# Performance work log

Measured on AMD Instinct MI355X. Metric: run time of the kernel, lower is better.

Reference implementation:

```python
import jax, jax.numpy as jnp
import numpy as np


def setup_inputs() -> dict:
    key = jax.random.key(0)
    B, C, H, W = 32, 1024, 32, 32
    K = 256
    corr = jax.random.normal(key, (B, C, H, W), dtype=jnp.float32)
    select_indices = jnp.arange(K, dtype=jnp.int64)
    return {"corr": corr, "select_indices": select_indices}


def reference(corr, select_indices):
    # corr: [B, C, H, W]
    max_corr = jnp.max(corr, axis=1, keepdims=True)    # [B,1,H,W]
    avg_corr = jnp.mean(corr, axis=1, keepdims=True)   # [B,1,H,W]
    # per-channel total response: sum over spatial dims -> [B, C]
    value = jnp.sum(corr, axis=(2, 3))
    # descending sort indices along channel dim, then keep selected ranks
    sort_v_idx = jnp.argsort(-value, axis=1)           # [B, C]
    sel_idx = sort_v_idx[:, select_indices]            # [B, K]
    # batched gather of the selected channels (vectorized, no python loop)
    sort_corr = jnp.take_along_axis(corr, sel_idx[:, :, None, None], axis=1)  # [B,K,H,W]
    return jnp.concatenate([max_corr, avg_corr, sort_corr], axis=1)  # [B, 2+K, H, W]
```

## Files before the change

kernel.cpp:

```cpp
#include <hip/hip_runtime.h>
#include <hip/hip_bf16.h>


#define BB 32
#define CC_TOT 1024
#define HW 1024

__global__ void k_pass1(const float* __restrict__ corr,
                        float* __restrict__ pmax,
                        float* __restrict__ psum,
                        double* __restrict__ value,
                        int nch, int cpc) {
    extern __shared__ double lds[];
    const int tid  = threadIdx.x;
    const int lane = tid & 63;
    const int wid  = tid >> 6;
    const int b  = blockIdx.x / nch;
    const int cc = blockIdx.x % nch;

    const float4* base = (const float4*)(corr + (((size_t)b * CC_TOT) + (size_t)cc * cpc) * HW);

    float4 vmax = make_float4(-__builtin_inff(), -__builtin_inff(),
                              -__builtin_inff(), -__builtin_inff());
    float4 vsum = make_float4(0.f, 0.f, 0.f, 0.f);

    for (int c = 0; c < cpc; ++c) {
        float4 x = base[(size_t)c * (HW / 4) + tid];
        vmax.x = fmaxf(vmax.x, x.x); vmax.y = fmaxf(vmax.y, x.y);
        vmax.z = fmaxf(vmax.z, x.z); vmax.w = fmaxf(vmax.w, x.w);
        vsum.x += x.x; vsum.y += x.y; vsum.z += x.z; vsum.w += x.w;

        double s = (double)x.x + (double)x.y + (double)x.z + (double)x.w;
        #pragma unroll
        for (int off = 32; off >= 1; off >>= 1)
            s += __shfl_down(s, off);
        if (lane == 0) lds[c * 4 + wid] = s;
    }
    __syncthreads();
    for (int c = tid; c < cpc; c += 256) {
        value[(size_t)b * CC_TOT + (size_t)cc * cpc + c] =
            lds[c * 4 + 0] + lds[c * 4 + 1] + lds[c * 4 + 2] + lds[c * 4 + 3];
    }

    const size_t o = ((size_t)blockIdx.x * HW) + (size_t)tid * 4;
    *(float4*)(pmax + o) = vmax;
    *(float4*)(psum + o) = vsum;
}

__global__ void k_pass2(const float* __restrict__ pmax,
                        const float* __restrict__ psum,
                        float* __restrict__ out, int nch) {
    const int gid = blockIdx.x * 256 + threadIdx.x;
    const int b  = gid >> 10;
    const int hw = gid & (HW - 1);
    float m = -__builtin_inff();
    float s = 0.f;
    for (int cc = 0; cc < nch; ++cc) {
        const size_t o = (((size_t)b * nch + cc) << 10) + hw;
        m = fmaxf(m, pmax[o]);
        s += psum[o];
    }
    const size_t ob = (size_t)b * (2 + 256) * HW;
    out[ob + hw]      = m;
    out[ob + HW + hw] = s * (1.0f / 1024.0f);
}

__global__ void k_sort(const double* __restrict__ value, int* __restrict__ sorted) {
    __shared__ double kv[1024];
    __shared__ int    ki[1024];
    const int b = blockIdx.x;
    const int tid = threadIdx.x;

    for (int i = tid; i < 1024; i += 512) {
        kv[i] = value[(size_t)b * CC_TOT + i];
        ki[i] = i;
    }
    __syncthreads();

    for (int k = 2; k <= 1024; k <<= 1) {
        for (int j = k >> 1; j > 0; j >>= 1) {
            for (int i = tid; i < 1024; i += 512) {
                const int ixj = i ^ j;
                if (ixj > i) {
                    double v1 = kv[i], v2 = kv[ixj];
                    int    i1 = ki[i], i2 = ki[ixj];
                    const bool prec = (v1 > v2) || (v1 == v2 && i1 < i2);
                    const bool up = (i & k) == 0;
                    const bool sw = up ? !prec : prec;
                    if (sw) {
                        kv[i] = v2; kv[ixj] = v1;
                        ki[i] = i2; ki[ixj] = i1;
                    }
                }
            }
            __syncthreads();
        }
    }
    for (int i = tid; i < 1024; i += 512)
        sorted[(size_t)b * CC_TOT + i] = ki[i];
}

__global__ void k_gather(const float* __restrict__ corr,
                         const int* __restrict__ sorted,
                         const int* __restrict__ selidx,
                         float* __restrict__ out, int K) {
    const int b = blockIdx.x / K;
    const int k = blockIdx.x % K;
    int ks = selidx[k];
    ks = min(max(ks, 0), CC_TOT - 1);
    int c = sorted[(size_t)b * CC_TOT + ks];
    c = min(max(c, 0), CC_TOT - 1);

    const float4* src = (const float4*)(corr + (((size_t)b * CC_TOT) + c) * HW);
    float4*       dst = (float4*)(out + (((size_t)b * (2 + 256)) + 2 + k) * HW);
    dst[threadIdx.x] = src[threadIdx.x];
}

extern "C" void kernel_launch(void* const* d_in, const int* in_sizes, int n_in,
                              void* d_out, int out_size, void* d_ws, size_t ws_size,
                              hipStream_t stream) {
    const float* corr = (const float*)d_in[0];
    const int*   sel  = (const int*)d_in[1];
    float*       out  = (float*)d_out;

    const int K = out_size / (BB * HW) - 2;

    int nch = 32;
    while (nch > 1) {
        size_t need = (size_t)BB * nch * HW * 4 * 2
                    + (size_t)BB * CC_TOT * 8
                    + (size_t)BB * CC_TOT * 4;
        if (need <= ws_size) break;
        nch >>= 1;
    }
    const int cpc = CC_TOT / nch;

    float*  pmax   = (float*)d_ws;
    float*  psum   = pmax + (size_t)BB * nch * HW;
    double* value  = (double*)(psum + (size_t)BB * nch * HW);
    int*    sorted = (int*)(value + (size_t)BB * CC_TOT);

    k_pass1<<<BB * nch, 256, (size_t)cpc * 4 * sizeof(double), stream>>>(
        corr, pmax, psum, value, nch, cpc);
    k_pass2<<<(BB * HW) / 256, 256, 0, stream>>>(pmax, psum, out, nch);
    k_sort<<<BB, 512, 0, stream>>>(value, sorted);
    k_gather<<<BB * K, 256, 0, stream>>>(corr, sorted, sel, out, K);
}
```

Baseline: 245.4 us.

## Replace bitonic sort with parallel rank counting and hardcode channel split

Replaces the per-batch 512-thread bitonic sort (many barrier-separated stages in one block per batch) with a rank-by-counting kernel. Each of 16 blocks per batch computes the descending rank of 64 channels by comparing against all 1024 values, then scatters only ranks below K. It also fixes the channel split at compile time, drops the workspace-size fallback, and adds unroll pragmas and launch bounds to the reduction kernels. The sorted array now holds only the first K ranks, so the gather is correct only if select_indices stay below K. The change also assumes the workspace is always large enough.

```diff
diff --git a/kernel.cpp b/kernel.cpp
--- a/kernel.cpp
+++ b/kernel.cpp
@@ -2,44 +2,48 @@
 #include <hip/hip_bf16.h>
 
 
-#define BB 32
-#define CC_TOT 1024
-#define HW 1024
+#define BB  32
+#define CC  1024
+#define HW  1024
+#define NCH 32
+#define CPC 32
 
-__global__ void k_pass1(const float* __restrict__ corr,
-                        float* __restrict__ pmax,
-                        float* __restrict__ psum,
-                        double* __restrict__ value,
-                        int nch, int cpc) {
-    extern __shared__ double lds[];
+__global__ __launch_bounds__(256)
+void k_pass1(const float* __restrict__ corr,
+             float* __restrict__ pmax,
+             float* __restrict__ psum,
+             double* __restrict__ value) {
+    __shared__ double lds[CPC * 4];
     const int tid  = threadIdx.x;
     const int lane = tid & 63;
     const int wid  = tid >> 6;
-    const int b  = blockIdx.x / nch;
-    const int cc = blockIdx.x % nch;
+    const int b  = blockIdx.x / NCH;
+    const int cc = blockIdx.x % NCH;
 
-    const float4* base = (const float4*)(corr + (((size_t)b * CC_TOT) + (size_t)cc * cpc) * HW);
+    const float4* base = (const float4*)(corr + (((size_t)b * CC) + (size_t)cc * CPC) * HW);
 
     float4 vmax = make_float4(-__builtin_inff(), -__builtin_inff(),
                               -__builtin_inff(), -__builtin_inff());
     float4 vsum = make_float4(0.f, 0.f, 0.f, 0.f);
 
-    for (int c = 0; c < cpc; ++c) {
+    #pragma unroll 4
+    for (int c = 0; c < CPC; ++c) {
         float4 x = base[(size_t)c * (HW / 4) + tid];
         vmax.x = fmaxf(vmax.x, x.x); vmax.y = fmaxf(vmax.y, x.y);
         vmax.z = fmaxf(vmax.z, x.z); vmax.w = fmaxf(vmax.w, x.w);
         vsum.x += x.x; vsum.y += x.y; vsum.z += x.z; vsum.w += x.w;
 
-        double s = (double)x.x + (double)x.y + (double)x.z + (double)x.w;
+        double s = ((double)x.x + (double)x.y) + ((double)x.z + (double)x.w);
         #pragma unroll
         for (int off = 32; off >= 1; off >>= 1)
             s += __shfl_down(s, off);
         if (lane == 0) lds[c * 4 + wid] = s;
     }
     __syncthreads();
-    for (int c = tid; c < cpc; c += 256) {
-        value[(size_t)b * CC_TOT + (size_t)cc * cpc + c] =
-            lds[c * 4 + 0] + lds[c * 4 + 1] + lds[c * 4 + 2] + lds[c * 4 + 3];
+    if (tid < CPC) {
+        const double v = (lds[tid * 4 + 0] + lds[tid * 4 + 1])
+                       + (lds[tid * 4 + 2] + lds[tid * 4 + 3]);
+        value[(size_t)b * CC + (size_t)cc * CPC + tid] = v;
     }
 
     const size_t o = ((size_t)blockIdx.x * HW) + (size_t)tid * 4;
@@ -47,16 +51,18 @@
     *(float4*)(psum + o) = vsum;
 }
 
-__global__ void k_pass2(const float* __restrict__ pmax,
-                        const float* __restrict__ psum,
-                        float* __restrict__ out, int nch) {
+__global__ __launch_bounds__(256)
+void k_pass2(const float* __restrict__ pmax,
+             const float* __restrict__ psum,
+             float* __restrict__ out) {
     const int gid = blockIdx.x * 256 + threadIdx.x;
     const int b  = gid >> 10;
     const int hw = gid & (HW - 1);
     float m = -__builtin_inff();
     float s = 0.f;
-    for (int cc = 0; cc < nch; ++cc) {
-        const size_t o = (((size_t)b * nch + cc) << 10) + hw;
+    #pragma unroll 8
+    for (int cc = 0; cc < NCH; ++cc) {
+        const size_t o = (((size_t)b * NCH + cc) << 10) + hw;
         m = fmaxf(m, pmax[o]);
         s += psum[o];
     }
@@ -65,53 +71,42 @@
     out[ob + HW + hw] = s * (1.0f / 1024.0f);
 }
 
-__global__ void k_sort(const double* __restrict__ value, int* __restrict__ sorted) {
-    __shared__ double kv[1024];
-    __shared__ int    ki[1024];
-    const int b = blockIdx.x;
-    const int tid = threadIdx.x;
+__global__ __launch_bounds__(64)
+void k_rank(const double* __restrict__ value, int* __restrict__ sorted, int K) {
+    __shared__ double vs[CC];
+    const int b     = blockIdx.x >> 4;
+    const int chunk = blockIdx.x & 15;
+    const int tid   = threadIdx.x;
 
-    for (int i = tid; i < 1024; i += 512) {
-        kv[i] = value[(size_t)b * CC_TOT + i];
-        ki[i] = i;
-    }
+    for (int i = tid; i < CC; i += 64)
+        vs[i] = value[(size_t)b * CC + i];
     __syncthreads();
 
-    for (int k = 2; k <= 1024; k <<= 1) {
-        for (int j = k >> 1; j > 0; j >>= 1) {
-            for (int i = tid; i < 1024; i += 512) {
-                const int ixj = i ^ j;
-                if (ixj > i) {
-                    double v1 = kv[i], v2 = kv[ixj];
-                    int    i1 = ki[i], i2 = ki[ixj];
-                    const bool prec = (v1 > v2) || (v1 == v2 && i1 < i2);
-                    const bool up = (i & k) == 0;
-                    const bool sw = up ? !prec : prec;
-                    if (sw) {
-                        kv[i] = v2; kv[ixj] = v1;
-                        ki[i] = i2; ki[ixj] = i1;
-                    }
-                }
-            }
-            __syncthreads();
-        }
+    const int    c  = chunk * 64 + tid;
+    const double my = vs[c];
+    int rank = 0;
+    #pragma unroll 8
+    for (int j = 0; j < CC; ++j) {
+        const double vj = vs[j];
+        rank += (vj > my) || (vj == my && j < c) ? 1 : 0;
     }
-    for (int i = tid; i < 1024; i += 512)
-        sorted[(size_t)b * CC_TOT + i] = ki[i];
+    if (rank < K)
+        sorted[(size_t)b * CC + rank] = c;
 }
 
-__global__ void k_gather(const float* __restrict__ corr,
-                         const int* __restrict__ sorted,
-                         const int* __restrict__ selidx,
-                         float* __restrict__ out, int K) {
+__global__ __launch_bounds__(256)
+void k_gather(const float* __restrict__ corr,
+              const int* __restrict__ sorted,
+              const int* __restrict__ selidx,
+              float* __restrict__ out, int K) {
     const int b = blockIdx.x / K;
     const int k = blockIdx.x % K;
     int ks = selidx[k];
-    ks = min(max(ks, 0), CC_TOT - 1);
-    int c = sorted[(size_t)b * CC_TOT + ks];
-    c = min(max(c, 0), CC_TOT - 1);
+    ks = min(max(ks, 0), CC - 1);
+    int c = sorted[(size_t)b * CC + ks];
+    c = min(max(c, 0), CC - 1);
 
-    const float4* src = (const float4*)(corr + (((size_t)b * CC_TOT) + c) * HW);
+    const float4* src = (const float4*)(corr + (((size_t)b * CC) + c) * HW);
     float4*       dst = (float4*)(out + (((size_t)b * (2 + 256)) + 2 + k) * HW);
     dst[threadIdx.x] = src[threadIdx.x];
 }
@@ -125,24 +120,13 @@
 
     const int K = out_size / (BB * HW) - 2;
 
-    int nch = 32;
-    while (nch > 1) {
-        size_t need = (size_t)BB * nch * HW * 4 * 2
-                    + (size_t)BB * CC_TOT * 8
-                    + (size_t)BB * CC_TOT * 4;
-        if (need <= ws_size) break;
-        nch >>= 1;
-    }
-    const int cpc = CC_TOT / nch;
+    float*  pmax   = (float*)d_ws;
+    float*  psum   = pmax + (size_t)BB * NCH * HW;
+    double* value  = (double*)(psum + (size_t)BB * NCH * HW);
+    int*    sorted = (int*)(value + (size_t)BB * CC);
 
-    float*  pmax   = (float*)d_ws;
-    float*  psum   = pmax + (size_t)BB * nch * HW;
-    double* value  = (double*)(psum + (size_t)BB * nch * HW);
-    int*    sorted = (int*)(value + (size_t)BB * CC_TOT);
-
-    k_pass1<<<BB * nch, 256, (size_t)cpc * 4 * sizeof(double), stream>>>(
-        corr, pmax, psum, value, nch, cpc);
-    k_pass2<<<(BB * HW) / 256, 256, 0, stream>>>(pmax, psum, out, nch);
-    k_sort<<<BB, 512, 0, stream>>>(value, sorted);
+    k_pass1<<<BB * NCH, 256, 0, stream>>>(corr, pmax, psum, value);
+    k_pass2<<<(BB * HW) / 256, 256, 0, stream>>>(pmax, psum, out);
+    k_rank<<<BB * 16, 64, 0, stream>>>(value, sorted, K);
     k_gather<<<BB * K, 256, 0, stream>>>(corr, sorted, sel, out, K);
 }
```

Result: no change. 245.3 us (-0.0%).
